# Kernel tuning notes

Measured on AMD Instinct MI355X. Metric: run time of the kernel, lower is better.

The kernel has to match this reference:

```python
import jax, jax.numpy as jnp
import numpy as np

N_EMBD = 1024
N_HEAD = 16
HEAD_DIM = N_EMBD // N_HEAD


def setup_inputs() -> dict:
    key = jax.random.key(0)
    k1, k2, k3, k4, k5 = jax.random.split(key, 5)
    B, T = 2, 2048
    x = jax.random.normal(k1, (B, T, N_EMBD), dtype=jnp.float32)
    # c_attn: Dense(3*n_embd), c_proj: Dense(n_embd); flax Dense kernel is [in, out]
    s = 0.02
    W_attn = jax.random.normal(k2, (N_EMBD, 3 * N_EMBD), dtype=jnp.float32) * s
    b_attn = jnp.zeros((3 * N_EMBD,), dtype=jnp.float32)
    W_proj = jax.random.normal(k3, (N_EMBD, N_EMBD), dtype=jnp.float32) * s
    b_proj = jnp.zeros((N_EMBD,), dtype=jnp.float32)
    return {"x": x, "W_attn": W_attn, "b_attn": b_attn, "W_proj": W_proj, "b_proj": b_proj}


def reference(x, W_attn, b_attn, W_proj, b_proj):
    B, T, C = x.shape
    qkv = x @ W_attn + b_attn                      # [B,T,3C]
    q, k, v = jnp.split(qkv, 3, axis=-1)
    q = q.reshape(B, T, N_HEAD, HEAD_DIM).transpose(0, 2, 1, 3)  # [B,H,T,D]
    k = k.reshape(B, T, N_HEAD, HEAD_DIM).transpose(0, 2, 1, 3)
    v = v.reshape(B, T, N_HEAD, HEAD_DIM).transpose(0, 2, 1, 3)
    scale = 1.0 / jnp.sqrt(jnp.float32(HEAD_DIM))
    att = jnp.einsum('bhqd,bhkd->bhqk', q, k) * scale            # [B,H,T,T]
    causal = jnp.tril(jnp.ones((T, T), dtype=bool))
    att = jnp.where(causal, att, -jnp.inf)
    att = jax.nn.softmax(att, axis=-1)
    y = jnp.einsum('bhqk,bhkd->bhqd', att, v)                    # [B,H,T,D]
    y = y.transpose(0, 2, 1, 3).reshape(B, T, C)
    return y @ W_proj + b_proj
```

## Files before the change

### kernel.cpp

```cpp
#include <hip/hip_runtime.h>
#include <hip/hip_bf16.h>
#include <math.h>

#define N_EMBD 1024
#define N_HEAD 16
#define HEAD_DIM 64
#define BSZ 2
#define TSEQ 2048
#define C3 (3 * N_EMBD)

typedef __attribute__((ext_vector_type(8))) short short8_t;
typedef __attribute__((ext_vector_type(4))) float f32x4;
typedef __attribute__((address_space(3))) unsigned int lds_u32;
typedef const __attribute__((address_space(1))) unsigned int glb_u32;

__device__ __forceinline__ unsigned short f2bf(float f) {
  return __builtin_bit_cast(unsigned short, __float2bfloat16(f));
}

__global__ __launch_bounds__(256) void conv_vec(
    const float* __restrict__ in, unsigned short* __restrict__ out, int n8)
{
  for (int i = blockIdx.x * blockDim.x + threadIdx.x; i < n8;
       i += gridDim.x * blockDim.x) {
    float4 a = ((const float4*)in)[2 * i];
    float4 b = ((const float4*)in)[2 * i + 1];
    union { unsigned short u[8]; uint4 q; } t;
    t.u[0] = f2bf(a.x); t.u[1] = f2bf(a.y); t.u[2] = f2bf(a.z); t.u[3] = f2bf(a.w);
    t.u[4] = f2bf(b.x); t.u[5] = f2bf(b.y); t.u[6] = f2bf(b.z); t.u[7] = f2bf(b.w);
    ((uint4*)out)[i] = t.q;
  }
}

__global__ __launch_bounds__(256) void conv_transpose(
    const float* __restrict__ in, unsigned short* __restrict__ out, int K, int N)
{
  __shared__ float tile[32][33];
  const int bk = blockIdx.y * 32, bn = blockIdx.x * 32;
  const int r = threadIdx.x >> 3, c4 = (threadIdx.x & 7) * 4;
  *(float4*)&tile[r][c4] = *(const float4*)(in + (size_t)(bk + r) * N + bn + c4);
  __syncthreads();
  union { unsigned short u[4]; uint2 q; } t;
#pragma unroll
  for (int j = 0; j < 4; ++j) t.u[j] = f2bf(tile[c4 + j][r]);
  *(uint2*)(out + (size_t)(bn + r) * K + bk + c4) = t.q;
}

__global__ __launch_bounds__(256) void conv_vT(
    const unsigned short* __restrict__ qkv, unsigned short* __restrict__ vt)
{
  __shared__ unsigned short tile[32][36];
  const int t0 = blockIdx.x * 32;
  const int d0 = blockIdx.y * 32;
  const int bh = blockIdx.z;
  const int b = bh >> 4, h = bh & 15;
  const int r = threadIdx.x >> 3, c4 = (threadIdx.x & 7) * 4;
  const unsigned short* src =
      qkv + ((size_t)b * TSEQ + t0 + r) * C3 + 2 * N_EMBD + h * HEAD_DIM + d0 + c4;
  *(uint2*)&tile[r][c4] = *(const uint2*)src;
  __syncthreads();
  union { unsigned short u[4]; uint2 q; } o;
#pragma unroll
  for (int j = 0; j < 4; ++j) o.u[j] = tile[c4 + j][r];
  *(uint2*)(vt + ((size_t)bh * HEAD_DIM + d0 + r) * TSEQ + t0 + c4) = o.q;
}

template <typename OUT_T>
__global__ __launch_bounds__(256) void gemm_mfma(
    const unsigned short* __restrict__ A,
    const unsigned short* __restrict__ Bt,
    const float* __restrict__ bias,
    OUT_T* __restrict__ C, int M, int N, int K)
{
  constexpr int BM = 128, BN = 128, BK = 32;
  __shared__ __align__(16) unsigned short As[BM * BK];
  __shared__ __align__(16) unsigned short Bs[BN * BK];

  const int tid = threadIdx.x;
  const int l = tid & 63;
  const int g = l >> 4, c = l & 15;
  const int w = tid >> 6;
  const int wr = w >> 1, wc = w & 1;
  const int bm = blockIdx.y * BM, bn = blockIdx.x * BN;

  f32x4 acc[4][4];
#pragma unroll
  for (int i = 0; i < 4; i++)
#pragma unroll
    for (int j = 0; j < 4; j++) acc[i][j] = (f32x4){0.f, 0.f, 0.f, 0.f};

  int srow[2], skq[2];
#pragma unroll
  for (int i = 0; i < 2; i++) {
    int seg = i * 256 + tid;
    srow[i] = seg >> 2;
    skq[i] = (seg & 3) ^ (srow[i] & 3);
  }

  for (int k0 = 0; k0 < K; k0 += BK) {
    __syncthreads();
#pragma unroll
    for (int i = 0; i < 2; i++) {
      int seg = i * 256 + tid;
      __builtin_amdgcn_global_load_lds(
          (glb_u32*)(A + (size_t)(bm + srow[i]) * K + k0 + skq[i] * 8),
          (lds_u32*)((char*)As + seg * 16), 16, 0, 0);
      __builtin_amdgcn_global_load_lds(
          (glb_u32*)(Bt + (size_t)(bn + srow[i]) * K + k0 + skq[i] * 8),
          (lds_u32*)((char*)Bs + seg * 16), 16, 0, 0);
    }
    __syncthreads();

    short8_t af[4], bf[4];
#pragma unroll
    for (int mi = 0; mi < 4; mi++) {
      int row = wr * 64 + mi * 16 + c;
      af[mi] = *(const short8_t*)((char*)As + row * 64 + ((g * 16) ^ ((row & 3) << 4)));
    }
#pragma unroll
    for (int ni = 0; ni < 4; ni++) {
      int row = wc * 64 + ni * 16 + c;
      bf[ni] = *(const short8_t*)((char*)Bs + row * 64 + ((g * 16) ^ ((row & 3) << 4)));
    }
    __builtin_amdgcn_s_setprio(1);
#pragma unroll
    for (int mi = 0; mi < 4; mi++)
#pragma unroll
      for (int ni = 0; ni < 4; ni++)
        acc[mi][ni] = __builtin_amdgcn_mfma_f32_16x16x32_bf16(af[mi], bf[ni], acc[mi][ni], 0, 0, 0);
    __builtin_amdgcn_s_setprio(0);
  }

  float bv[4];
#pragma unroll
  for (int ni = 0; ni < 4; ni++) bv[ni] = bias[bn + wc * 64 + ni * 16 + c];
#pragma unroll
  for (int mi = 0; mi < 4; mi++)
#pragma unroll
    for (int j = 0; j < 4; j++) {
      int row = bm + wr * 64 + mi * 16 + g * 4 + j;
      OUT_T* cp = C + (size_t)row * N + bn + wc * 64 + c;
#pragma unroll
      for (int ni = 0; ni < 4; ni++) {
        float v = acc[mi][ni][j] + bv[ni];
        if constexpr (sizeof(OUT_T) == 2)
          *(unsigned short*)(cp + ni * 16) = f2bf(v);
        else
          *(float*)(cp + ni * 16) = v;
      }
    }
}

__global__ __launch_bounds__(256) void attn_mfma(
    const unsigned short* __restrict__ qkv,
    const unsigned short* __restrict__ vt,
    unsigned short* __restrict__ y)
{
  const int l = threadIdx.x & 63;
  const int w = threadIdx.x >> 6;
  const int b = blockIdx.z, h = blockIdx.y;
  const int pair = blockIdx.x;
  const int g = l >> 4;
  const int c = l & 15;

  __shared__ __align__(16) unsigned short Ks[64 * 64];
  __shared__ __align__(16) unsigned short Vt[64 * 64];
  __shared__ __align__(16) unsigned short Ps[4][16 * 64];

  const unsigned short* base = qkv + (size_t)b * TSEQ * C3;
  const unsigned short* vbase = vt + (size_t)(b * N_HEAD + h) * HEAD_DIM * TSEQ;
  const float SCALE_LOG2E = 0.125f * 1.44269504f;

#pragma unroll 1
  for (int half = 0; half < 2; ++half) {
    const int tile = half == 0 ? (31 - pair) : pair;
    const int r0 = tile * 64;
    const int qr0 = r0 + w * 16;

    short8_t qf[2];
    {
      const unsigned short* qp = base + (size_t)(qr0 + c) * C3 + h * HEAD_DIM + g * 8;
      qf[0] = *(const short8_t*)(qp);
      qf[1] = *(const short8_t*)(qp + 32);
    }

    f32x4 o[4];
    float m[4], ld[4];
#pragma unroll
    for (int dt = 0; dt < 4; ++dt) o[dt] = (f32x4){0.f, 0.f, 0.f, 0.f};
#pragma unroll
    for (int r = 0; r < 4; ++r) { m[r] = -1e30f; ld[r] = 0.f; }

    const int nch = tile + 1;
#pragma unroll 1
    for (int ci = 0; ci < nch; ++ci) {
      const int k0 = ci * 64;
      __syncthreads();
#pragma unroll
      for (int s = 0; s < 2; ++s) {
        int seg = threadIdx.x + s * 256;
        int kr = seg >> 3, d8 = (seg & 7) * 8;
        uint4 t = *(const uint4*)(base + (size_t)(k0 + kr) * C3 + N_EMBD + h * HEAD_DIM + d8);
        *(uint4*)((char*)Ks + kr * 128 + ((d8 * 2) ^ ((kr & 7) << 4))) = t;
      }
#pragma unroll
      for (int s = 0; s < 2; ++s) {
        int seg = threadIdx.x + s * 256;
        int dr = seg >> 3, k8 = (seg & 7) * 8;
        uint4 t = *(const uint4*)(vbase + (size_t)dr * TSEQ + k0 + k8);
        *(uint4*)((char*)Vt + dr * 128 + ((k8 * 2) ^ ((dr & 7) << 4))) = t;
      }
      __syncthreads();
      if (k0 > qr0 + 15) continue;

      f32x4 st[4];
      __builtin_amdgcn_s_setprio(1);
#pragma unroll
      for (int kt = 0; kt < 4; ++kt) {
        const int row = kt * 16 + c;
        short8_t kf0 = *(const short8_t*)((const char*)Ks + row * 128 + ((g * 16) ^ ((row & 7) << 4)));
        short8_t kf1 = *(const short8_t*)((const char*)Ks + row * 128 + ((64 + g * 16) ^ ((row & 7) << 4)));
        f32x4 a2 = (f32x4){0.f, 0.f, 0.f, 0.f};
        a2 = __builtin_amdgcn_mfma_f32_16x16x32_bf16(qf[0], kf0, a2, 0, 0, 0);
        a2 = __builtin_amdgcn_mfma_f32_16x16x32_bf16(qf[1], kf1, a2, 0, 0, 0);
        st[kt] = a2;
      }
      __builtin_amdgcn_s_setprio(0);

      const bool full = (k0 + 63 <= qr0);
#pragma unroll
      for (int r = 0; r < 4; ++r) {
        const int qg = qr0 + g * 4 + r;
        float mx = -1e30f;
#pragma unroll
        for (int kt = 0; kt < 4; ++kt) {
          float s = st[kt][r] * SCALE_LOG2E;
          if (!full) { int kg = k0 + kt * 16 + c; if (kg > qg) s = -1e30f; }
          st[kt][r] = s;
          mx = fmaxf(mx, s);
        }
        mx = fmaxf(mx, __shfl_xor(mx, 1));
        mx = fmaxf(mx, __shfl_xor(mx, 2));
        mx = fmaxf(mx, __shfl_xor(mx, 4));
        mx = fmaxf(mx, __shfl_xor(mx, 8));
        float mnew = fmaxf(m[r], mx);
        float corr = exp2f(m[r] - mnew);
        m[r] = mnew;
        float rs = 0.f;
        const int row = g * 4 + r;
#pragma unroll
        for (int kt = 0; kt < 4; ++kt) {
          float p = exp2f(st[kt][r] - mnew);
          rs += p;
          *(unsigned short*)((char*)Ps[w] + row * 128 +
                             (((kt * 16 + c) * 2) ^ ((row & 7) << 4))) = f2bf(p);
        }
        rs += __shfl_xor(rs, 1);
        rs += __shfl_xor(rs, 2);
        rs += __shfl_xor(rs, 4);
        rs += __shfl_xor(rs, 8);
        ld[r] = ld[r] * corr + rs;
#pragma unroll
        for (int dt = 0; dt < 4; ++dt) o[dt][r] *= corr;
      }
      short8_t pf[2];
#pragma unroll
      for (int kc = 0; kc < 2; ++kc)
        pf[kc] = *(const short8_t*)((const char*)Ps[w] + c * 128 +
                                    ((64 * kc + g * 16) ^ ((c & 7) << 4)));
      __builtin_amdgcn_s_setprio(1);
#pragma unroll
      for (int dt = 0; dt < 4; ++dt) {
        const int row = dt * 16 + c;
#pragma unroll
        for (int kc = 0; kc < 2; ++kc) {
          short8_t vf = *(const short8_t*)((const char*)Vt + row * 128 +
                                           ((64 * kc + g * 16) ^ ((row & 7) << 4)));
          o[dt] = __builtin_amdgcn_mfma_f32_16x16x32_bf16(pf[kc], vf, o[dt], 0, 0, 0);
        }
      }
      __builtin_amdgcn_s_setprio(0);
    }
#pragma unroll
    for (int r = 0; r < 4; ++r) {
      float inv = 1.f / ld[r];
      const size_t rowoff = ((size_t)b * TSEQ + qr0 + g * 4 + r) * N_EMBD + h * HEAD_DIM;
#pragma unroll
      for (int dt = 0; dt < 4; ++dt)
        y[rowoff + dt * 16 + c] = f2bf(o[dt][r] * inv);
    }
  }
}

extern "C" void kernel_launch(void* const* d_in, const int* in_sizes, int n_in,
                              void* d_out, int out_size, void* d_ws, size_t ws_size,
                              hipStream_t stream) {
  const float* x      = (const float*)d_in[0];
  const float* W_attn = (const float*)d_in[1];
  const float* b_attn = (const float*)d_in[2];
  const float* W_proj = (const float*)d_in[3];
  const float* b_proj = (const float*)d_in[4];
  float* out = (float*)d_out;

  const int M = BSZ * TSEQ;

  unsigned short* xb   = (unsigned short*)d_ws;
  unsigned short* Wta  = xb + (size_t)M * N_EMBD;
  unsigned short* Wtp  = Wta + (size_t)C3 * N_EMBD;
  unsigned short* qkvb = Wtp + (size_t)N_EMBD * N_EMBD;
  unsigned short* yatt = qkvb + (size_t)M * C3;
  unsigned short* vtb  = yatt + (size_t)M * N_EMBD;

  conv_vec<<<2048, 256, 0, stream>>>(x, xb, M * N_EMBD / 8);
  conv_transpose<<<dim3(C3 / 32, N_EMBD / 32), 256, 0, stream>>>(W_attn, Wta, N_EMBD, C3);
  conv_transpose<<<dim3(N_EMBD / 32, N_EMBD / 32), 256, 0, stream>>>(W_proj, Wtp, N_EMBD, N_EMBD);

  gemm_mfma<unsigned short><<<dim3(C3 / 128, M / 128), 256, 0, stream>>>(
      xb, Wta, b_attn, qkvb, M, C3, N_EMBD);

  conv_vT<<<dim3(TSEQ / 32, HEAD_DIM / 32, BSZ * N_HEAD), 256, 0, stream>>>(qkvb, vtb);

  attn_mfma<<<dim3(TSEQ / 128, N_HEAD, BSZ), 256, 0, stream>>>(qkvb, vtb, yatt);

  gemm_mfma<float><<<dim3(N_EMBD / 128, M / 128), 256, 0, stream>>>(
      yatt, Wtp, b_proj, out, M, N_EMBD, N_EMBD);
}
```

Baseline: 233.3 us.

## Split KV chunks across two wave groups per attention block and merge

The attention block grows to 512 threads, forming two groups of four waves. Each group processes alternate 64-key chunks with its own K/V LDS buffers. The partial softmax state (o, m, l) is then merged through shared memory before writing the output. The aim is to double the waves per query tile, since the grid of 512 blocks leaves the GPU lightly occupied and each block otherwise walks the causal chunks serially. In exchange it adds a merge step with extra barriers, more LDS, and possible out-of-range K/V loads when the chunk count is odd.

```diff
diff --git a/kernel.cpp b/kernel.cpp
--- a/kernel.cpp
+++ b/kernel.cpp
@@ -151,21 +151,28 @@
     }
 }
 
-__global__ __launch_bounds__(256) void attn_mfma(
+__global__ __launch_bounds__(512) void attn_mfma(
     const unsigned short* __restrict__ qkv,
     const unsigned short* __restrict__ vt,
     unsigned short* __restrict__ y)
 {
-  const int l = threadIdx.x & 63;
-  const int w = threadIdx.x >> 6;
+  const int tid = threadIdx.x;
+  const int l = tid & 63;
+  const int w = tid >> 6;
+  const int g2 = w >> 2;
+  const int wg = w & 3;
+  const int tid2 = tid & 255;
   const int b = blockIdx.z, h = blockIdx.y;
   const int pair = blockIdx.x;
   const int g = l >> 4;
   const int c = l & 15;
 
-  __shared__ __align__(16) unsigned short Ks[64 * 64];
-  __shared__ __align__(16) unsigned short Vt[64 * 64];
-  __shared__ __align__(16) unsigned short Ps[4][16 * 64];
+  __shared__ __align__(16) unsigned short S[24576];
+  unsigned short* Ksg = S + g2 * 8192;
+  unsigned short* Vsg = S + 4096 + g2 * 8192;
+  unsigned short* Psw = S + 16384 + w * 1024;
+  float* osc = (float*)(S + 8192);
+  float* mlsc = (float*)(S + 16384 + 4 * 1024);
 
   const unsigned short* base = qkv + (size_t)b * TSEQ * C3;
   const unsigned short* vbase = vt + (size_t)(b * N_HEAD + h) * HEAD_DIM * TSEQ;
@@ -174,8 +181,7 @@
 #pragma unroll 1
   for (int half = 0; half < 2; ++half) {
     const int tile = half == 0 ? (31 - pair) : pair;
-    const int r0 = tile * 64;
-    const int qr0 = r0 + w * 16;
+    const int qr0 = tile * 64 + wg * 16;
 
     short8_t qf[2];
     {
@@ -192,23 +198,25 @@
     for (int r = 0; r < 4; ++r) { m[r] = -1e30f; ld[r] = 0.f; }
 
     const int nch = tile + 1;
+    const int iters = (nch + 1) >> 1;
 #pragma unroll 1
-    for (int ci = 0; ci < nch; ++ci) {
+    for (int i = 0; i < iters; ++i) {
+      const int ci = 2 * i + g2;
       const int k0 = ci * 64;
       __syncthreads();
 #pragma unroll
       for (int s = 0; s < 2; ++s) {
-        int seg = threadIdx.x + s * 256;
+        int seg = tid2 + s * 256;
         int kr = seg >> 3, d8 = (seg & 7) * 8;
         uint4 t = *(const uint4*)(base + (size_t)(k0 + kr) * C3 + N_EMBD + h * HEAD_DIM + d8);
-        *(uint4*)((char*)Ks + kr * 128 + ((d8 * 2) ^ ((kr & 7) << 4))) = t;
+        *(uint4*)((char*)Ksg + kr * 128 + ((d8 * 2) ^ ((kr & 7) << 4))) = t;
       }
 #pragma unroll
       for (int s = 0; s < 2; ++s) {
-        int seg = threadIdx.x + s * 256;
+        int seg = tid2 + s * 256;
         int dr = seg >> 3, k8 = (seg & 7) * 8;
         uint4 t = *(const uint4*)(vbase + (size_t)dr * TSEQ + k0 + k8);
-        *(uint4*)((char*)Vt + dr * 128 + ((k8 * 2) ^ ((dr & 7) << 4))) = t;
+        *(uint4*)((char*)Vsg + dr * 128 + ((k8 * 2) ^ ((dr & 7) << 4))) = t;
       }
       __syncthreads();
       if (k0 > qr0 + 15) continue;
@@ -218,8 +226,8 @@
 #pragma unroll
       for (int kt = 0; kt < 4; ++kt) {
         const int row = kt * 16 + c;
-        short8_t kf0 = *(const short8_t*)((const char*)Ks + row * 128 + ((g * 16) ^ ((row & 7) << 4)));
-        short8_t kf1 = *(const short8_t*)((const char*)Ks + row * 128 + ((64 + g * 16) ^ ((row & 7) << 4)));
+        short8_t kf0 = *(const short8_t*)((const char*)Ksg + row * 128 + ((g * 16) ^ ((row & 7) << 4)));
+        short8_t kf1 = *(const short8_t*)((const char*)Ksg + row * 128 + ((64 + g * 16) ^ ((row & 7) << 4)));
         f32x4 a2 = (f32x4){0.f, 0.f, 0.f, 0.f};
         a2 = __builtin_amdgcn_mfma_f32_16x16x32_bf16(qf[0], kf0, a2, 0, 0, 0);
         a2 = __builtin_amdgcn_mfma_f32_16x16x32_bf16(qf[1], kf1, a2, 0, 0, 0);
@@ -252,7 +260,7 @@
         for (int kt = 0; kt < 4; ++kt) {
           float p = exp2f(st[kt][r] - mnew);
           rs += p;
-          *(unsigned short*)((char*)Ps[w] + row * 128 +
+          *(unsigned short*)((char*)Psw + row * 128 +
                              (((kt * 16 + c) * 2) ^ ((row & 7) << 4))) = f2bf(p);
         }
         rs += __shfl_xor(rs, 1);
@@ -266,7 +274,7 @@
       short8_t pf[2];
 #pragma unroll
       for (int kc = 0; kc < 2; ++kc)
-        pf[kc] = *(const short8_t*)((const char*)Ps[w] + c * 128 +
+        pf[kc] = *(const short8_t*)((const char*)Psw + c * 128 +
                                     ((64 * kc + g * 16) ^ ((c & 7) << 4)));
       __builtin_amdgcn_s_setprio(1);
 #pragma unroll
@@ -274,20 +282,46 @@
         const int row = dt * 16 + c;
 #pragma unroll
         for (int kc = 0; kc < 2; ++kc) {
-          short8_t vf = *(const short8_t*)((const char*)Vt + row * 128 +
+          short8_t vf = *(const short8_t*)((const char*)Vsg + row * 128 +
                                            ((64 * kc + g * 16) ^ ((row & 7) << 4)));
           o[dt] = __builtin_amdgcn_mfma_f32_16x16x32_bf16(pf[kc], vf, o[dt], 0, 0, 0);
         }
       }
       __builtin_amdgcn_s_setprio(0);
     }
-#pragma unroll
-    for (int r = 0; r < 4; ++r) {
-      float inv = 1.f / ld[r];
-      const size_t rowoff = ((size_t)b * TSEQ + qr0 + g * 4 + r) * N_EMBD + h * HEAD_DIM;
-#pragma unroll
-      for (int dt = 0; dt < 4; ++dt)
-        y[rowoff + dt * 16 + c] = f2bf(o[dt][r] * inv);
+
+    __syncthreads();
+    if (g2 == 1) {
+      float* ow = osc + wg * 1024;
+      float* ml = mlsc + wg * 512;
+#pragma unroll
+      for (int r = 0; r < 4; ++r) {
+        const int row = g * 4 + r;
+        ml[row] = m[r];
+        ml[16 + row] = ld[r];
+#pragma unroll
+        for (int dt = 0; dt < 4; ++dt)
+          ow[row * 64 + dt * 16 + c] = o[dt][r];
+      }
+    }
+    __syncthreads();
+    if (g2 == 0) {
+      float* ow = osc + wg * 1024;
+      float* ml = mlsc + wg * 512;
+#pragma unroll
+      for (int r = 0; r < 4; ++r) {
+        const int row = g * 4 + r;
+        float m1 = ml[row], l1 = ml[16 + row];
+        float ms = fmaxf(m[r], m1);
+        float c0 = exp2f(m[r] - ms);
+        float c1 = exp2f(m1 - ms);
+        float inv = 1.f / (ld[r] * c0 + l1 * c1);
+        const size_t rowoff = ((size_t)b * TSEQ + qr0 + row) * N_EMBD + h * HEAD_DIM;
+#pragma unroll
+        for (int dt = 0; dt < 4; ++dt)
+          y[rowoff + dt * 16 + c] =
+              f2bf((o[dt][r] * c0 + ow[row * 64 + dt * 16 + c] * c1) * inv);
+      }
     }
   }
 }
@@ -320,7 +354,7 @@
 
   conv_vT<<<dim3(TSEQ / 32, HEAD_DIM / 32, BSZ * N_HEAD), 256, 0, stream>>>(qkvb, vtb);
 
-  attn_mfma<<<dim3(TSEQ / 128, N_HEAD, BSZ), 256, 0, stream>>>(qkvb, vtb, yatt);
+  attn_mfma<<<dim3(TSEQ / 128, N_HEAD, BSZ), 512, 0, stream>>>(qkvb, vtb, yatt);
 
   gemm_mfma<float><<<dim3(N_EMBD / 128, M / 128), 256, 0, stream>>>(
       yatt, Wtp, b_proj, out, M, N_EMBD, N_EMBD);
```

After: 218.3 us. -6.4%, faster.
